# Kernel optimization log

Measured on AMD Instinct MI355X. Metric: run time of the kernel, lower is better.

The kernel has to match this reference:

```python
import jax, jax.numpy as jnp
import numpy as np

B, S, T, E = 16, 512, 4096, 256  # batch, phone count, frame count, embed dim


def _pe(t, e):
    # sinusoidal positional encoding table [t, e], matches PositionalEncoding
    pos = jnp.arange(t, dtype=jnp.float32)[:, None]
    div = jnp.exp(jnp.arange(0, e, 2, dtype=jnp.float32) * (-np.log(10000.0) / e))
    pe = jnp.zeros((t, e), jnp.float32)
    pe = pe.at[:, 0::2].set(jnp.sin(pos * div))
    pe = pe.at[:, 1::2].set(jnp.cos(pos * div))
    return pe


def setup_inputs() -> dict:
    key = jax.random.key(0)
    ks = jax.random.split(key, 8)
    encoder_out = jax.random.normal(ks[0], (B, S, E), jnp.float32)
    # text_phone with adjacent values guaranteed distinct (even pos in [0,29), odd in [30,59))
    base = jax.random.randint(ks[1], (B, S), 0, 29)
    off = (jnp.arange(S) % 2) * 30
    text_phone = (base + off[None, :]).astype(jnp.int64)
    dur = T // S
    align_phone = jnp.repeat(text_phone, dur, axis=1)  # [B, T], consistent alignment
    pitch = jax.random.normal(ks[2], (B, T, 1), jnp.float32)
    beats = jax.random.randint(ks[3], (B, T, 1), 0, 2).astype(jnp.int64)
    # learned parameters
    W_pitch = jax.random.normal(ks[4], (1, E), jnp.float32) * 0.02   # fc_pitch
    b_pitch = jnp.zeros((E,), jnp.float32)
    emb_beats = jax.random.normal(ks[5], (2, E), jnp.float32) * 0.02
    W_pos = jax.random.normal(ks[6], (E, E), jnp.float32) * (1.0 / np.sqrt(E))  # fc_pos
    b_pos = jnp.zeros((E,), jnp.float32)
    return dict(encoder_out=encoder_out, align_phone=align_phone, text_phone=text_phone,
                pitch=pitch, beats=beats, W_pitch=W_pitch, b_pitch=b_pitch,
                emb_beats=emb_beats, W_pos=W_pos, b_pos=b_pos)


def _align_indices(align_phone, text_phone):
    # Vectorized version of the serial aligner loop: per batch, an index into
    # encoder_out that stays while align_phone matches the current text phone
    # and advances by 1 otherwise.
    Bb, Ss = text_phone.shape
    barange = jnp.arange(Bb)

    def step(idx, a_j):
        before = text_phone[barange, idx]
        new = jnp.where(a_j == before, idx, jnp.minimum(idx + 1, Ss - 1))
        return new, new

    idx0 = jnp.zeros((Bb,), jnp.int32)
    _, rest = jax.lax.scan(step, idx0, align_phone[:, 1:].T)  # [T-1, B]
    return jnp.concatenate([idx0[None, :], rest], axis=0).T  # [B, T]


def reference(encoder_out, align_phone, text_phone, pitch, beats,
              W_pitch, b_pitch, emb_beats, W_pos, b_pos):
    idx = _align_indices(align_phone, text_phone)                       # [B, T]
    aligner_out = jnp.take_along_axis(encoder_out, idx[:, :, None].astype(jnp.int32), axis=1)  # [B, T, E]
    pitch_emb = pitch @ W_pitch + b_pitch                               # fc_pitch(pitch)
    beat_emb = emb_beats[beats[..., 0]]                                 # emb_beats(beats.squeeze(-1))
    # pos(aligner_out.transpose(0,1)) then transpose back; dropout is identity in eval
    pos_encode = aligner_out + _pe(aligner_out.shape[1], aligner_out.shape[2])[None, :, :]
    pos_out = pos_encode @ W_pos + b_pos                                # fc_pos
    return aligner_out + pitch_emb + beat_emb + pos_out
```

## Files before the change

### kernel.cpp

```cpp
#include <hip/hip_runtime.h>
#include <hip/hip_bf16.h>
#include <math.h>

constexpr int B_ = 16, S_ = 512, T_ = 4096, E_ = 256;

typedef __attribute__((ext_vector_type(8))) short short8;
typedef __attribute__((ext_vector_type(4))) float f32x4;

constexpr size_t FLAGS_OFF = 0;
constexpr size_t WT_OFF    = 4096;

#define NEGC (-0.035977892f)

__device__ __forceinline__ unsigned pk_bf16(float a, float b) {
    __hip_bfloat162 h = __float22bfloat162_rn(make_float2(a, b));
    return *(unsigned*)&h;
}
__device__ __forceinline__ short bf16s(float x) {
    unsigned u = __float_as_uint(x);
    u += 0x7FFFu + ((u >> 16) & 1u);
    return (short)(u >> 16);
}

__global__ __launch_bounds__(256) void k_prep(
    const int* __restrict__ align, const int* __restrict__ text,
    const float* __restrict__ W,
    int* __restrict__ flags, short* __restrict__ wt)
{
    const int bid = blockIdx.x, tid = threadIdx.x;
    if (bid < 32) {
        __shared__ int f;
        if (tid == 0) f = 0;
        __syncthreads();
        const int base = (bid * 256 + tid) * 8;
        const int4 a0 = *(const int4*)(align + base);
        const int4 a1 = *(const int4*)(align + base + 4);
        const int av[8] = {a0.x, a0.y, a0.z, a0.w, a1.x, a1.y, a1.z, a1.w};
        int bad = 0;
#pragma unroll
        for (int m = 0; m < 8; ++m) {
            const int id = base + m;
            const int t = id & (T_ - 1), b = id >> 12;
            if (t > 0) {
                const int prev = (t - 1) >> 3;
                const int expct = (av[m] == text[b * S_ + prev]) ? prev : min(prev + 1, S_ - 1);
                if ((t >> 3) != expct) bad = 1;
            }
        }
        if (bad) f = 1;
        __syncthreads();
        if (tid == 0) flags[bid] = f;
    } else {
        const int kb = (bid - 32) * 16;
        short8 v0, v1;
#pragma unroll
        for (int j = 0; j < 8; ++j) v0[j] = bf16s(W[(kb + j) * E_ + tid]);
#pragma unroll
        for (int j = 0; j < 8; ++j) v1[j] = bf16s(W[(kb + 8 + j) * E_ + tid]);
        *(short8*)(wt + tid * E_ + kb)     = v0;
        *(short8*)(wt + tid * E_ + kb + 8) = v1;
    }
}

__global__ __launch_bounds__(256, 3) void k_fused(
    const float* __restrict__ enc, const short* __restrict__ wt,
    const float* __restrict__ bpos,
    const float* __restrict__ pitch, const int* __restrict__ beats,
    const float* __restrict__ wpitch, const float* __restrict__ bpitch,
    const float* __restrict__ embb,
    const float* __restrict__ W, const int* __restrict__ align,
    const int* __restrict__ text, const int* __restrict__ flags,
    float* __restrict__ out)
{
    __shared__ __align__(16) short As[64 * 256];
    __shared__ __align__(16) short Bs[32 * 256];
    __shared__ float pl[4 * 256];

    const int tid = threadIdx.x;
    const int i0 = blockIdx.x * 4;
    const int n0 = blockIdx.y * 32;
    const int t0base = i0 * 8;

    const bool fb = __any(flags[tid & 31] != 0);
    if (fb) {
        int (*idxl)[32] = (int(*)[32])As;
        if (tid < 16) {
            int i = 0;
            const int b = tid;
            if (i0 == 0) idxl[b][0] = 0;
            for (int t = 1; t < t0base + 32; ++t) {
                if (align[b * T_ + t] != text[b * S_ + i]) i = min(i + 1, S_ - 1);
                if (t >= t0base) idxl[b][t - t0base] = i;
            }
        }
        __syncthreads();
#pragma unroll
        for (int rr = 0; rr < 2; ++rr) {
            const int r = tid * 2 + rr;
            const int bq = r >> 5, tt = r & 31;
            const int t = t0base + tt;
            const int i = idxl[bq][tt];
            const float* erow = enc + (size_t)(bq * S_ + i) * E_;
            const float p = pitch[(size_t)bq * T_ + t];
            const int bt = beats[(size_t)bq * T_ + t];
            for (int cc = 0; cc < 32; ++cc) {
                const int col = n0 + cc;
                float acc = 0.f;
                for (int k2 = 0; k2 < 128; ++k2) {
                    const float dd = __expf((float)(2 * k2) * NEGC);
                    float s, c;
                    __sincosf((float)t * dd, &s, &c);
                    acc += (erow[2 * k2] + s) * W[(2 * k2) * E_ + col]
                         + (erow[2 * k2 + 1] + c) * W[(2 * k2 + 1) * E_ + col];
                }
                out[((size_t)bq * T_ + t) * E_ + col] =
                    erow[col] + acc + bpos[col] + p * wpitch[col] + bpitch[col]
                    + (bt ? embb[E_ + col] : embb[col]);
            }
        }
        return;
    }

    {
        const int r = tid >> 3, c8 = tid & 7;
        const short* bp = wt + (size_t)(n0 + r) * E_;
#pragma unroll
        for (int jj = 0; jj < 4; ++jj) {
            const int seg = c8 + 8 * jj;
            short8 v = *(const short8*)(bp + seg * 8);
            *(short8*)&Bs[(r * 256 + seg * 8) ^ ((r & 7) << 3)] = v;
        }
    }
    {
        const int r = tid >> 3, c8 = tid & 7;
        const float tf = (float)(t0base + r);
#pragma unroll
        for (int jj = 0; jj < 4; ++jj) {
            const int seg = c8 * 4 + jj;
            union { short8 v; unsigned u[4]; } cv;
#pragma unroll
            for (int m = 0; m < 4; ++m) {
                const int j2 = seg * 4 + m;
                const float d = __expf((float)(2 * j2) * NEGC);
                float s, c;
                __sincosf(tf * d, &s, &c);
                cv.u[m] = pk_bf16(s, c);
            }
            *(short8*)&As[(r * 256 + seg * 8) ^ ((r & 7) << 3)] = cv.v;
        }
    }
    __syncthreads();

    const int wid = tid >> 6, lane = tid & 63;
    const int q = lane >> 4, c = lane & 15;

    {
        const int tq = wid >> 1, nqp = wid & 1;
        const int ar = tq * 16 + c;
        const int br = nqp * 16 + c;
        f32x4 p = {0.f, 0.f, 0.f, 0.f};
#pragma unroll
        for (int ks = 0; ks < 8; ++ks) {
            const int kidx = ks * 32 + q * 8;
            short8 a = *(const short8*)&As[(ar * 256 + kidx) ^ ((ar & 7) << 3)];
            short8 b = *(const short8*)&Bs[(br * 256 + kidx) ^ ((br & 7) << 3)];
            p = __builtin_amdgcn_mfma_f32_16x16x32_bf16(a, b, p, 0, 0, 0);
        }
#pragma unroll
        for (int rr = 0; rr < 4; ++rr)
            pl[(tq * 2 + nqp) * 256 + (q * 4 + rr) * 16 + c] = p[rr];
    }
    __syncthreads();

    {
        const int r = tid >> 2, c4 = tid & 3;
        const float* ap = enc + (size_t)((r >> 2) * S_ + i0 + (r & 3)) * E_;
#pragma unroll
        for (int jj = 0; jj < 8; ++jj) {
            const int seg = c4 + 4 * jj;
            float4 f0 = *(const float4*)(ap + seg * 8);
            float4 f1 = *(const float4*)(ap + seg * 8 + 4);
            union { short8 v; unsigned u[4]; } cv;
            cv.u[0] = pk_bf16(f0.x, f0.y);
            cv.u[1] = pk_bf16(f0.z, f0.w);
            cv.u[2] = pk_bf16(f1.x, f1.y);
            cv.u[3] = pk_bf16(f1.z, f1.w);
            *(short8*)&As[(r * 256 + seg * 8) ^ ((r & 7) << 3)] = cv.v;
        }
    }
    __syncthreads();

    const int mq = wid >> 1, nq = wid & 1;
    const int ra0 = mq * 32 + c, ra1 = ra0 + 16;
    const int rb = nq * 16 + c;
    f32x4 acc0 = {0.f, 0.f, 0.f, 0.f}, acc1 = {0.f, 0.f, 0.f, 0.f};
#pragma unroll
    for (int ks = 0; ks < 8; ++ks) {
        const int kidx = ks * 32 + q * 8;
        short8 a0 = *(const short8*)&As[(ra0 * 256 + kidx) ^ ((ra0 & 7) << 3)];
        short8 a1 = *(const short8*)&As[(ra1 * 256 + kidx) ^ ((ra1 & 7) << 3)];
        short8 b  = *(const short8*)&Bs[(rb * 256 + kidx) ^ ((rb & 7) << 3)];
        acc0 = __builtin_amdgcn_mfma_f32_16x16x32_bf16(a0, b, acc0, 0, 0, 0);
        acc1 = __builtin_amdgcn_mfma_f32_16x16x32_bf16(a1, b, acc1, 0, 0, 0);
    }

    const int c8q = tid & 7, rgrp = tid >> 3;
    const int j = rgrp & 3;
    const int gc = n0 + 4 * c8q;
    f32x4 pv[8];
#pragma unroll
    for (int d = 0; d < 8; ++d) {
        const int tl = j * 8 + d;
        pv[d] = *(const f32x4*)&pl[((tl >> 4) * 2 + (c8q >> 2)) * 256
                                   + (tl & 15) * 16 + ((4 * c8q) & 15)];
    }
    const f32x4 wp4 = *(const f32x4*)(wpitch + gc);
    const f32x4 cst = *(const f32x4*)(bpitch + gc) + *(const f32x4*)(bpos + gc);
    const f32x4 be0 = *(const f32x4*)(embb + gc);
    const f32x4 be1 = *(const f32x4*)(embb + E_ + gc);
    __syncthreads();

    float* ew = (float*)As;
#pragma unroll
    for (int rr = 0; rr < 4; ++rr) {
        ew[(mq * 32 + q * 4 + rr) * 36 + nq * 16 + c]      = acc0[rr];
        ew[(mq * 32 + 16 + q * 4 + rr) * 36 + nq * 16 + c] = acc1[rr];
    }
    __syncthreads();

#pragma unroll
    for (int p = 0; p < 2; ++p) {
        const int row = rgrp + 32 * p;
        const int bq = row >> 2;
        const size_t prow = (size_t)bq * T_ + t0base + j * 8;
        const float4 pi0 = *(const float4*)(pitch + prow);
        const float4 pi1 = *(const float4*)(pitch + prow + 4);
        const int4  bt0 = *(const int4*)(beats + prow);
        const int4  bt1 = *(const int4*)(beats + prow + 4);
        const f32x4 e4  = *(const f32x4*)(enc + (size_t)(bq * S_ + i0 + j) * E_ + gc);
        const f32x4 ewv = *(const f32x4*)&ew[row * 36 + 4 * c8q];
        const f32x4 base = ewv + e4 + cst;
        const float pp[8] = {pi0.x, pi0.y, pi0.z, pi0.w, pi1.x, pi1.y, pi1.z, pi1.w};
        const int   bb[8] = {bt0.x, bt0.y, bt0.z, bt0.w, bt1.x, bt1.y, bt1.z, bt1.w};
#pragma unroll
        for (int d = 0; d < 8; ++d) {
            const f32x4 be = bb[d] ? be1 : be0;
            f32x4 o = base + pv[d] + pp[d] * wp4 + be;
            __builtin_nontemporal_store(o, (f32x4*)(out + (prow + d) * E_ + gc));
        }
    }
}

extern "C" void kernel_launch(void* const* d_in, const int* in_sizes, int n_in,
                              void* d_out, int out_size, void* d_ws, size_t ws_size,
                              hipStream_t stream) {
    const float* enc    = (const float*)d_in[0];
    const int*   align  = (const int*)  d_in[1];
    const int*   text   = (const int*)  d_in[2];
    const float* pitch  = (const float*)d_in[3];
    const int*   beats  = (const int*)  d_in[4];
    const float* wpitch = (const float*)d_in[5];
    const float* bpitch = (const float*)d_in[6];
    const float* embb   = (const float*)d_in[7];
    const float* wpos   = (const float*)d_in[8];
    const float* bpos   = (const float*)d_in[9];
    float* out = (float*)d_out;

    char* ws = (char*)d_ws;
    int*   flags = (int*)  (ws + FLAGS_OFF);
    short* wt    = (short*)(ws + WT_OFF);

    hipLaunchKernelGGL(k_prep, dim3(48), dim3(256), 0, stream,
                       align, text, wpos, flags, wt);
    hipLaunchKernelGGL(k_fused, dim3(S_ / 4, 8), dim3(256), 0, stream,
                       enc, wt, bpos, pitch, beats, wpitch, bpitch, embb,
                       wpos, align, text, flags, out);
}
```

Before: 25.58 us.

## Process two column chunks per block to reuse staged encoder and PE tiles

Each block now covers 64 output columns in two 32-column chunks, so the bf16 encoder tile and the sinusoidal PE tile are built once and reused across both chunks. The grid is halved along the column axis and launch bounds drop to 2 blocks per SM. A raw barrier that skips the vmem wait is used in the second chunk to avoid stalling on the outstanding nontemporal stores. This cuts redundant global loads and sin/cos work but enlarges shared memory, lowers occupancy, and serialises the two chunks inside each block.

Measured after the change: 25.47 us. Within noise of the previous version (-0.4%).

```diff
diff --git a/kernel.cpp b/kernel.cpp
--- a/kernel.cpp
+++ b/kernel.cpp
@@ -20,6 +20,12 @@
     unsigned u = __float_as_uint(x);
     u += 0x7FFFu + ((u >> 16) & 1u);
     return (short)(u >> 16);
+}
+
+__device__ __forceinline__ void rawbar() {
+    asm volatile("s_waitcnt lgkmcnt(0)" ::: "memory");
+    __builtin_amdgcn_s_barrier();
+    __builtin_amdgcn_sched_barrier(0);
 }
 
 __global__ __launch_bounds__(256) void k_prep(
@@ -62,7 +68,7 @@
     }
 }
 
-__global__ __launch_bounds__(256, 3) void k_fused(
+__global__ __launch_bounds__(256, 2) void k_fused(
     const float* __restrict__ enc, const short* __restrict__ wt,
     const float* __restrict__ bpos,
     const float* __restrict__ pitch, const int* __restrict__ beats,
@@ -73,12 +79,13 @@
     float* __restrict__ out)
 {
     __shared__ __align__(16) short As[64 * 256];
+    __shared__ __align__(16) short Ps[32 * 256];
     __shared__ __align__(16) short Bs[32 * 256];
-    __shared__ float pl[4 * 256];
+    __shared__ __align__(16) float scratch[64 * 36];
 
     const int tid = threadIdx.x;
     const int i0 = blockIdx.x * 4;
-    const int n0 = blockIdx.y * 32;
+    const int n0base = blockIdx.y * 64;
     const int t0base = i0 * 8;
 
     const bool fb = __any(flags[tid & 31] != 0);
@@ -103,8 +110,8 @@
             const float* erow = enc + (size_t)(bq * S_ + i) * E_;
             const float p = pitch[(size_t)bq * T_ + t];
             const int bt = beats[(size_t)bq * T_ + t];
-            for (int cc = 0; cc < 32; ++cc) {
-                const int col = n0 + cc;
+            for (int cc = 0; cc < 64; ++cc) {
+                const int col = n0base + cc;
                 float acc = 0.f;
                 for (int k2 = 0; k2 < 128; ++k2) {
                     const float dd = __expf((float)(2 * k2) * NEGC);
@@ -122,57 +129,6 @@
     }
 
     {
-        const int r = tid >> 3, c8 = tid & 7;
-        const short* bp = wt + (size_t)(n0 + r) * E_;
-#pragma unroll
-        for (int jj = 0; jj < 4; ++jj) {
-            const int seg = c8 + 8 * jj;
-            short8 v = *(const short8*)(bp + seg * 8);
-            *(short8*)&Bs[(r * 256 + seg * 8) ^ ((r & 7) << 3)] = v;
-        }
-    }
-    {
-        const int r = tid >> 3, c8 = tid & 7;
-        const float tf = (float)(t0base + r);
-#pragma unroll
-        for (int jj = 0; jj < 4; ++jj) {
-            const int seg = c8 * 4 + jj;
-            union { short8 v; unsigned u[4]; } cv;
-#pragma unroll
-            for (int m = 0; m < 4; ++m) {
-                const int j2 = seg * 4 + m;
-                const float d = __expf((float)(2 * j2) * NEGC);
-                float s, c;
-                __sincosf(tf * d, &s, &c);
-                cv.u[m] = pk_bf16(s, c);
-            }
-            *(short8*)&As[(r * 256 + seg * 8) ^ ((r & 7) << 3)] = cv.v;
-        }
-    }
-    __syncthreads();
-
-    const int wid = tid >> 6, lane = tid & 63;
-    const int q = lane >> 4, c = lane & 15;
-
-    {
-        const int tq = wid >> 1, nqp = wid & 1;
-        const int ar = tq * 16 + c;
-        const int br = nqp * 16 + c;
-        f32x4 p = {0.f, 0.f, 0.f, 0.f};
-#pragma unroll
-        for (int ks = 0; ks < 8; ++ks) {
-            const int kidx = ks * 32 + q * 8;
-            short8 a = *(const short8*)&As[(ar * 256 + kidx) ^ ((ar & 7) << 3)];
-            short8 b = *(const short8*)&Bs[(br * 256 + kidx) ^ ((br & 7) << 3)];
-            p = __builtin_amdgcn_mfma_f32_16x16x32_bf16(a, b, p, 0, 0, 0);
-        }
-#pragma unroll
-        for (int rr = 0; rr < 4; ++rr)
-            pl[(tq * 2 + nqp) * 256 + (q * 4 + rr) * 16 + c] = p[rr];
-    }
-    __syncthreads();
-
-    {
         const int r = tid >> 2, c4 = tid & 3;
         const float* ap = enc + (size_t)((r >> 2) * S_ + i0 + (r & 3)) * E_;
 #pragma unroll
@@ -188,66 +144,123 @@
             *(short8*)&As[(r * 256 + seg * 8) ^ ((r & 7) << 3)] = cv.v;
         }
     }
-    __syncthreads();
-
-    const int mq = wid >> 1, nq = wid & 1;
-    const int ra0 = mq * 32 + c, ra1 = ra0 + 16;
-    const int rb = nq * 16 + c;
-    f32x4 acc0 = {0.f, 0.f, 0.f, 0.f}, acc1 = {0.f, 0.f, 0.f, 0.f};
-#pragma unroll
-    for (int ks = 0; ks < 8; ++ks) {
-        const int kidx = ks * 32 + q * 8;
-        short8 a0 = *(const short8*)&As[(ra0 * 256 + kidx) ^ ((ra0 & 7) << 3)];
-        short8 a1 = *(const short8*)&As[(ra1 * 256 + kidx) ^ ((ra1 & 7) << 3)];
-        short8 b  = *(const short8*)&Bs[(rb * 256 + kidx) ^ ((rb & 7) << 3)];
-        acc0 = __builtin_amdgcn_mfma_f32_16x16x32_bf16(a0, b, acc0, 0, 0, 0);
-        acc1 = __builtin_amdgcn_mfma_f32_16x16x32_bf16(a1, b, acc1, 0, 0, 0);
-    }
-
+    {
+        const int r = tid >> 3, c8 = tid & 7;
+        const float tf = (float)(t0base + r);
+#pragma unroll
+        for (int jj = 0; jj < 4; ++jj) {
+            const int seg = c8 * 4 + jj;
+            union { short8 v; unsigned u[4]; } cv;
+#pragma unroll
+            for (int m = 0; m < 4; ++m) {
+                const int j2 = seg * 4 + m;
+                const float d = __expf((float)(2 * j2) * NEGC);
+                float s, c;
+                __sincosf(tf * d, &s, &c);
+                cv.u[m] = pk_bf16(s, c);
+            }
+            *(short8*)&Ps[(r * 256 + seg * 8) ^ ((r & 7) << 3)] = cv.v;
+        }
+    }
+
+    const int wid = tid >> 6, lane = tid & 63;
+    const int q = lane >> 4, c = lane & 15;
     const int c8q = tid & 7, rgrp = tid >> 3;
     const int j = rgrp & 3;
-    const int gc = n0 + 4 * c8q;
-    f32x4 pv[8];
-#pragma unroll
-    for (int d = 0; d < 8; ++d) {
-        const int tl = j * 8 + d;
-        pv[d] = *(const f32x4*)&pl[((tl >> 4) * 2 + (c8q >> 2)) * 256
-                                   + (tl & 15) * 16 + ((4 * c8q) & 15)];
-    }
-    const f32x4 wp4 = *(const f32x4*)(wpitch + gc);
-    const f32x4 cst = *(const f32x4*)(bpitch + gc) + *(const f32x4*)(bpos + gc);
-    const f32x4 be0 = *(const f32x4*)(embb + gc);
-    const f32x4 be1 = *(const f32x4*)(embb + E_ + gc);
-    __syncthreads();
-
-    float* ew = (float*)As;
-#pragma unroll
-    for (int rr = 0; rr < 4; ++rr) {
-        ew[(mq * 32 + q * 4 + rr) * 36 + nq * 16 + c]      = acc0[rr];
-        ew[(mq * 32 + 16 + q * 4 + rr) * 36 + nq * 16 + c] = acc1[rr];
-    }
-    __syncthreads();
-
-#pragma unroll
-    for (int p = 0; p < 2; ++p) {
-        const int row = rgrp + 32 * p;
-        const int bq = row >> 2;
-        const size_t prow = (size_t)bq * T_ + t0base + j * 8;
-        const float4 pi0 = *(const float4*)(pitch + prow);
-        const float4 pi1 = *(const float4*)(pitch + prow + 4);
-        const int4  bt0 = *(const int4*)(beats + prow);
-        const int4  bt1 = *(const int4*)(beats + prow + 4);
-        const f32x4 e4  = *(const f32x4*)(enc + (size_t)(bq * S_ + i0 + j) * E_ + gc);
-        const f32x4 ewv = *(const f32x4*)&ew[row * 36 + 4 * c8q];
-        const f32x4 base = ewv + e4 + cst;
-        const float pp[8] = {pi0.x, pi0.y, pi0.z, pi0.w, pi1.x, pi1.y, pi1.z, pi1.w};
-        const int   bb[8] = {bt0.x, bt0.y, bt0.z, bt0.w, bt1.x, bt1.y, bt1.z, bt1.w};
+    float* const pl = scratch;
+    float* const ew = scratch;
+
+#pragma unroll
+    for (int chunk = 0; chunk < 2; ++chunk) {
+        const int n0 = n0base + chunk * 32;
+
+        {
+            const int r = tid >> 3, cc8 = tid & 7;
+            const short* bp = wt + (size_t)(n0 + r) * E_;
+#pragma unroll
+            for (int jj = 0; jj < 4; ++jj) {
+                const int seg = cc8 + 8 * jj;
+                short8 v = *(const short8*)(bp + seg * 8);
+                *(short8*)&Bs[(r * 256 + seg * 8) ^ ((r & 7) << 3)] = v;
+            }
+        }
+        if (chunk == 0) __syncthreads(); else rawbar();
+
+        {
+            const int tq = wid >> 1, nqp = wid & 1;
+            const int ar = tq * 16 + c;
+            const int br = nqp * 16 + c;
+            f32x4 p = {0.f, 0.f, 0.f, 0.f};
+#pragma unroll
+            for (int ks = 0; ks < 8; ++ks) {
+                const int kidx = ks * 32 + q * 8;
+                short8 a = *(const short8*)&Ps[(ar * 256 + kidx) ^ ((ar & 7) << 3)];
+                short8 b = *(const short8*)&Bs[(br * 256 + kidx) ^ ((br & 7) << 3)];
+                p = __builtin_amdgcn_mfma_f32_16x16x32_bf16(a, b, p, 0, 0, 0);
+            }
+#pragma unroll
+            for (int rr = 0; rr < 4; ++rr)
+                pl[(tq * 2 + nqp) * 256 + (q * 4 + rr) * 16 + c] = p[rr];
+        }
+        if (chunk == 0) __syncthreads(); else rawbar();
+
+        const int mq = wid >> 1, nq = wid & 1;
+        const int ra0 = mq * 32 + c, ra1 = ra0 + 16;
+        const int rb = nq * 16 + c;
+        f32x4 acc0 = {0.f, 0.f, 0.f, 0.f}, acc1 = {0.f, 0.f, 0.f, 0.f};
+#pragma unroll
+        for (int ks = 0; ks < 8; ++ks) {
+            const int kidx = ks * 32 + q * 8;
+            short8 a0 = *(const short8*)&As[(ra0 * 256 + kidx) ^ ((ra0 & 7) << 3)];
+            short8 a1 = *(const short8*)&As[(ra1 * 256 + kidx) ^ ((ra1 & 7) << 3)];
+            short8 b  = *(const short8*)&Bs[(rb * 256 + kidx) ^ ((rb & 7) << 3)];
+            acc0 = __builtin_amdgcn_mfma_f32_16x16x32_bf16(a0, b, acc0, 0, 0, 0);
+            acc1 = __builtin_amdgcn_mfma_f32_16x16x32_bf16(a1, b, acc1, 0, 0, 0);
+        }
+
+        const int gc = n0 + 4 * c8q;
+        f32x4 pv[8];
 #pragma unroll
         for (int d = 0; d < 8; ++d) {
-            const f32x4 be = bb[d] ? be1 : be0;
-            f32x4 o = base + pv[d] + pp[d] * wp4 + be;
-            __builtin_nontemporal_store(o, (f32x4*)(out + (prow + d) * E_ + gc));
-        }
+            const int tl = j * 8 + d;
+            pv[d] = *(const f32x4*)&pl[((tl >> 4) * 2 + (c8q >> 2)) * 256
+                                       + (tl & 15) * 16 + ((4 * c8q) & 15)];
+        }
+        const f32x4 wp4 = *(const f32x4*)(wpitch + gc);
+        const f32x4 cst = *(const f32x4*)(bpitch + gc) + *(const f32x4*)(bpos + gc);
+        const f32x4 be0 = *(const f32x4*)(embb + gc);
+        const f32x4 be1 = *(const f32x4*)(embb + E_ + gc);
+        if (chunk == 0) __syncthreads(); else rawbar();
+
+#pragma unroll
+        for (int rr = 0; rr < 4; ++rr) {
+            ew[(mq * 32 + q * 4 + rr) * 36 + nq * 16 + c]      = acc0[rr];
+            ew[(mq * 32 + 16 + q * 4 + rr) * 36 + nq * 16 + c] = acc1[rr];
+        }
+        if (chunk == 0) __syncthreads(); else rawbar();
+
+#pragma unroll
+        for (int p = 0; p < 2; ++p) {
+            const int row = rgrp + 32 * p;
+            const int bq = row >> 2;
+            const size_t prow = (size_t)bq * T_ + t0base + j * 8;
+            const float4 pi0 = *(const float4*)(pitch + prow);
+            const float4 pi1 = *(const float4*)(pitch + prow + 4);
+            const int4  bt0 = *(const int4*)(beats + prow);
+            const int4  bt1 = *(const int4*)(beats + prow + 4);
+            const f32x4 e4  = *(const f32x4*)(enc + (size_t)(bq * S_ + i0 + j) * E_ + gc);
+            const f32x4 ewv = *(const f32x4*)&ew[row * 36 + 4 * c8q];
+            const f32x4 base = ewv + e4 + cst;
+            const float pp[8] = {pi0.x, pi0.y, pi0.z, pi0.w, pi1.x, pi1.y, pi1.z, pi1.w};
+            const int   bb[8] = {bt0.x, bt0.y, bt0.z, bt0.w, bt1.x, bt1.y, bt1.z, bt1.w};
+#pragma unroll
+            for (int d = 0; d < 8; ++d) {
+                const f32x4 be = bb[d] ? be1 : be0;
+                f32x4 o = base + pv[d] + pp[d] * wp4 + be;
+                __builtin_nontemporal_store(o, (f32x4*)(out + (prow + d) * E_ + gc));
+            }
+        }
+        if (chunk == 0) rawbar();
     }
 }
 
@@ -272,7 +285,7 @@
 
     hipLaunchKernelGGL(k_prep, dim3(48), dim3(256), 0, stream,
                        align, text, wpos, flags, wt);
-    hipLaunchKernelGGL(k_fused, dim3(S_ / 4, 8), dim3(256), 0, stream,
+    hipLaunchKernelGGL(k_fused, dim3(S_ / 4, 4), dim3(256), 0, stream,
                        enc, wt, bpos, pitch, beats, wpitch, bpitch, embb,
                        wpos, align, text, flags, out);
 }
```
